# Kernel optimization log

Hardware: AMD Instinct MI355X
Metric: run time of the kernel (lower is better)

## Reference

```python
import jax, jax.numpy as jnp
import numpy as np

N_MOLS = 2048       # number of molecules (segments)
BOND_FDIM = 14      # slice last BOND_FDIM columns of f_bonds
DEPTH = 3


def setup_inputs() -> dict:
    key = jax.random.key(0)
    ks = jax.random.split(key, 12)
    n_atoms, n_bonds = 65536, 131072
    atom_fdim, bond_total, hidden, max_nb = 133, 147, 256, 6
    atom_features = jax.random.normal(ks[0], (n_atoms, atom_fdim), jnp.float32)
    f_bonds = jax.random.normal(ks[1], (n_bonds, bond_total), jnp.float32)
    a2a = jax.random.randint(ks[2], (n_atoms, max_nb), 0, n_atoms, jnp.int32)
    a2b = jax.random.randint(ks[3], (n_atoms, max_nb), 0, n_bonds, jnp.int32)
    segment_ids = jnp.sort(jax.random.randint(ks[4], (n_atoms,), 0, N_MOLS, jnp.int32))
    s = 0.05
    Wi = jax.random.normal(ks[5], (atom_fdim, hidden), jnp.float32) * s
    bi = jax.random.normal(ks[6], (hidden,), jnp.float32) * s
    Wh = jax.random.normal(ks[7], (hidden + BOND_FDIM, hidden), jnp.float32) * s
    bh = jax.random.normal(ks[8], (hidden,), jnp.float32) * s
    Wo = jax.random.normal(ks[9], (atom_fdim + hidden, hidden), jnp.float32) * s
    bo = jax.random.normal(ks[10], (hidden,), jnp.float32) * s
    return {"atom_features": atom_features, "f_bonds": f_bonds, "a2a": a2a,
            "a2b": a2b, "segment_ids": segment_ids,
            "Wi": Wi, "bi": bi, "Wh": Wh, "bh": bh, "Wo": Wo, "bo": bo}


def reference(atom_features, f_bonds, a2a, a2b, segment_ids, Wi, bi, Wh, bh, Wo, bo):
    # W_i + ReLU
    inp = atom_features @ Wi + bi                      # [N, H]
    message = jax.nn.relu(inp)
    fb = f_bonds[:, -BOND_FDIM:]                       # slice last bond_fdim cols
    # depth-1 message passing steps
    for _ in range(DEPTH - 1):
        nei_a_sum = message[a2a].sum(axis=1)           # [N, H]   gather + sum
        nei_b_sum = fb[a2b].sum(axis=1)                # [N, Fb]  gather + sum
        # sum(concat) == concat(sums) over neighbor axis
        m = jnp.concatenate([nei_a_sum, nei_b_sum], axis=1) @ Wh + bh
        message = jax.nn.relu(inp + m)                 # dropout: eval mode (identity)
    # final atom readout
    a_message = message[a2a].sum(axis=1)               # [N, H]
    a_input = jnp.concatenate([atom_features, a_message], axis=1)
    atom_hiddens = jax.nn.relu(a_input @ Wo + bo)      # [N, H]
    # segment-mean pooling over molecules (empty segments -> zero vector)
    sums = jax.ops.segment_sum(atom_hiddens, segment_ids, num_segments=N_MOLS)
    counts = jax.ops.segment_sum(jnp.ones((atom_hiddens.shape[0],), atom_hiddens.dtype),
                                 segment_ids, num_segments=N_MOLS)
    vecs = jnp.where(counts[:, None] > 0, sums / jnp.maximum(counts, 1.0)[:, None], 0.0)
    return vecs
```

## Files before the change

kernel.cpp:

```cpp
#include <hip/hip_runtime.h>

#define N_ATOMS 65536
#define AF      133
#define BT      147
#define HID     256
#define NNB     6
#define NM      2048

#define KI   160
#define KB   32
#define KP   256
#define LSI  168
#define LSB  40
#define LSP  264

#define BM   32

typedef __attribute__((ext_vector_type(8))) short short8;
typedef __attribute__((ext_vector_type(4))) float f32x4;

__device__ __forceinline__ unsigned short f2bf(float f) {
    unsigned u = __builtin_bit_cast(unsigned, f);
    u += 0x7fffu + ((u >> 16) & 1u);
    return (unsigned short)(u >> 16);
}
__device__ __forceinline__ float bf2f(unsigned short s) {
    unsigned u = ((unsigned)s) << 16;
    return __builtin_bit_cast(float, u);
}

__device__ __forceinline__ size_t fidx(int K, int n, int k) {
    return ((size_t)(((n >> 4) * (K >> 5) + (k >> 5)) * 64
                     + (((k >> 3) & 3) << 4) + (n & 15)) << 3) + (k & 7);
}

__global__ __launch_bounds__(256) void k_prep_bond(const float* __restrict__ Wi,
                                                   const float* __restrict__ Wh,
                                                   const float* __restrict__ Wo,
                                                   const float* __restrict__ bi,
                                                   const float* __restrict__ bh,
                                                   const float* __restrict__ f_bonds,
                                                   const int* __restrict__ a2b,
                                                   unsigned short* __restrict__ Wi_f,
                                                   unsigned short* __restrict__ Wb_f,
                                                   unsigned short* __restrict__ Whm_f,
                                                   unsigned short* __restrict__ Woa_f,
                                                   unsigned short* __restrict__ Wom_f,
                                                   unsigned short* __restrict__ bondsum,
                                                   float* __restrict__ b_ih) {
    if (blockIdx.x < 256) {
        const int n = blockIdx.x;
        if (n == 0) b_ih[threadIdx.x] = bi[threadIdx.x] + bh[threadIdx.x];
        for (int k = threadIdx.x; k < KI; k += 256) {
            Wi_f[fidx(KI, n, k)]  = f2bf(k < AF ? Wi[k * HID + n] : 0.f);
            Woa_f[fidx(KI, n, k)] = f2bf(k < AF ? Wo[k * HID + n] : 0.f);
        }
        for (int k = threadIdx.x; k < KB; k += 256)
            Wb_f[fidx(KB, n, k)] = f2bf(k < 14 ? Wh[(HID + k) * HID + n] : 0.f);
        for (int k = threadIdx.x; k < KP; k += 256) {
            Whm_f[fidx(KP, n, k)] = f2bf(Wh[k * HID + n]);
            Wom_f[fidx(KP, n, k)] = f2bf(Wo[(AF + k) * HID + n]);
        }
    } else {
        const int id   = (blockIdx.x - 256) * 256 + threadIdx.x;
        const int atom = id >> 4;
        const int c    = id & 15;
        float s = 0.f;
        if (c < 14) {
            const int* nb = &a2b[atom * NNB];
#pragma unroll
            for (int t = 0; t < NNB; ++t)
                s += f_bonds[(size_t)nb[t] * BT + (BT - 14) + c];
        }
        bondsum[atom * 32 + c]      = f2bf(s);
        bondsum[atom * 32 + 16 + c] = 0;
    }
}

template<int K, int LS>
__device__ __forceinline__ void mfma_core_pf(const unsigned short* __restrict__ As,
                                             const unsigned short* __restrict__ Wt,
                                             f32x4 (&acc)[2][2], int cw, int lane) {
    constexpr int NK = K >> 5;
    const int lm = lane & 15, quad = lane >> 4;
    const short8* __restrict__ Wf = (const short8*)Wt;
    short8 bf[2][NK];
#pragma unroll
    for (int ks = 0; ks < NK; ++ks)
#pragma unroll
        for (int ct = 0; ct < 2; ++ct)
            bf[ct][ks] = Wf[(size_t)((cw * 2 + ct) * NK + ks) * 64 + lane];
#pragma unroll
    for (int ks = 0; ks < NK; ++ks) {
        short8 af[2];
#pragma unroll
        for (int rt = 0; rt < 2; ++rt)
            af[rt] = *(const short8*)&As[(rt * 16 + lm) * LS + ks * 32 + quad * 8];
#pragma unroll
        for (int rt = 0; rt < 2; ++rt)
#pragma unroll
            for (int ct = 0; ct < 2; ++ct)
                acc[rt][ct] = __builtin_amdgcn_mfma_f32_16x16x32_bf16(af[rt], bf[ct][ks], acc[rt][ct], 0, 0, 0);
    }
}

__device__ __forceinline__ void epi_to_lds(f32x4 (&acc)[2][2],
                                           const float* __restrict__ bias,
                                           bool relu_,
                                           unsigned short* __restrict__ E,
                                           int cw, int lane) {
    const int lm = lane & 15, quad = lane >> 4;
#pragma unroll
    for (int ct = 0; ct < 2; ++ct) {
        int col = cw * 32 + ct * 16 + lm;
        float bv = bias ? bias[col] : 0.f;
#pragma unroll
        for (int rt = 0; rt < 2; ++rt)
#pragma unroll
            for (int i = 0; i < 4; ++i) {
                float v = acc[rt][ct][i] + bv;
                if (relu_) v = fmaxf(v, 0.f);
                E[(rt * 16 + quad * 4 + i) * LSP + col] = f2bf(v);
            }
    }
}

template<int NT>
__device__ __forceinline__ void store_tile(unsigned short* __restrict__ dst, int base,
                                           const unsigned short* __restrict__ E, int tid) {
#pragma unroll
    for (int k = 0; k < BM * HID / (8 * NT); ++k) {
        int j = k * NT + tid;
        int r = j >> 5, g = j & 31;
        *(short8*)&dst[(size_t)(base + r) * HID + g * 8] = *(const short8*)&E[r * LSP + g * 8];
    }
}

__global__ __launch_bounds__(512, 6) void k_inp(const float* __restrict__ atom,
                                                const unsigned short* __restrict__ bondsum,
                                                const unsigned short* __restrict__ Wi_f,
                                                const unsigned short* __restrict__ Wb_f,
                                                const unsigned short* __restrict__ Whm_f,
                                                const unsigned short* __restrict__ Woa_f,
                                                const float* __restrict__ bi,
                                                const float* __restrict__ b_ih,
                                                const float* __restrict__ bo,
                                                unsigned short* __restrict__ P0,
                                                unsigned short* __restrict__ inp2,
                                                unsigned short* __restrict__ aw) {
    __shared__ unsigned short pool[BM * LSP * 2 + BM * LSB];
    unsigned short* X    = pool;
    unsigned short* work = pool + BM * LSP;
    unsigned short* bs   = pool + BM * LSP * 2;
    const int tid  = threadIdx.x;
    const int base = blockIdx.x * BM;

    for (int it = tid; it < BM * KI; it += 512) {
        int r = it / KI, c = it - r * KI;
        X[r * LSI + c] = f2bf(c < AF ? atom[(size_t)(base + r) * AF + c] : 0.f);
    }
    if (tid < BM * 4) {
        int r = tid >> 2, c = (tid & 3) * 8;
        *(short8*)&bs[r * LSB + c] = *(const short8*)&bondsum[(size_t)(base + r) * 32 + c];
    }
    __syncthreads();

    const int lane = tid & 63, cw = tid >> 6;
    f32x4 acc1[2][2] = {}, acc3[2][2] = {};
    mfma_core_pf<KI, LSI>(X, Wi_f, acc1, cw, lane);
    mfma_core_pf<KI, LSI>(X, Woa_f, acc3, cw, lane);
    __syncthreads();

    epi_to_lds(acc3, bo, false, X, cw, lane);
    epi_to_lds(acc1, bi, true, work, cw, lane);
    __syncthreads();

    store_tile<512>(aw, base, X, tid);
    f32x4 acc2[2][2] = {};
    mfma_core_pf<KP, LSP>(work, Whm_f, acc2, cw, lane);
    mfma_core_pf<KB, LSB>(bs, Wb_f, acc1, cw, lane);
    __syncthreads();

    epi_to_lds(acc2, nullptr, false, X, cw, lane);
    epi_to_lds(acc1, b_ih, false, work, cw, lane);
    __syncthreads();

    store_tile<512>(P0, base, X, tid);
    store_tile<512>(inp2, base, work, tid);
}

__global__ __launch_bounds__(512, 6) void k_it(const unsigned short* __restrict__ Pin,
                                               const unsigned short* __restrict__ base_,
                                               const int* __restrict__ a2a,
                                               const unsigned short* __restrict__ Wt,
                                               unsigned short* __restrict__ Pout) {
    __shared__ unsigned short mT[BM * LSP];
    __shared__ int nb_l[BM * NNB];
    const int tid  = threadIdx.x;
    const int base = blockIdx.x * BM;

    if (tid < BM * NNB) nb_l[tid] = a2a[base * NNB + tid];
    __syncthreads();

#pragma unroll
    for (int k = 0; k < 2; ++k) {
        int j = k * 512 + tid;
        int r = j >> 5, g = j & 31;
        const int* nb = &nb_l[r * NNB];
        float s[8] = {};
#pragma unroll
        for (int t = 0; t < NNB; ++t) {
            short8 u = *(const short8*)&Pin[(size_t)nb[t] * HID + g * 8];
#pragma unroll
            for (int q = 0; q < 8; ++q) s[q] += bf2f((unsigned short)u[q]);
        }
        short8 b = *(const short8*)&base_[(size_t)(base + r) * HID + g * 8];
        short8 o;
#pragma unroll
        for (int q = 0; q < 8; ++q)
            o[q] = (short)f2bf(fmaxf(s[q] + bf2f((unsigned short)b[q]), 0.f));
        *(short8*)&mT[r * LSP + g * 8] = o;
    }
    __syncthreads();

    const int lane = tid & 63, cw = tid >> 6;
    f32x4 acc[2][2] = {};
    mfma_core_pf<KP, LSP>(mT, Wt, acc, cw, lane);
    __syncthreads();
    epi_to_lds(acc, nullptr, false, mT, cw, lane);
    __syncthreads();
    store_tile<512>(Pout, base, mT, tid);
}

__global__ __launch_bounds__(256, 8) void k_gseg(const unsigned short* __restrict__ P,
                                                 const unsigned short* __restrict__ aw,
                                                 const int* __restrict__ a2a,
                                                 const int* __restrict__ seg,
                                                 float* __restrict__ out) {
    const int m = blockIdx.x;
    __shared__ int lohi[2];
    __shared__ float red[8 * 256];
    if (threadIdx.x == 0) {
        int lo = 0, hi = N_ATOMS;
        while (lo < hi) { int mid = (lo + hi) >> 1; if (seg[mid] < m) lo = mid + 1; else hi = mid; }
        lohi[0] = lo;
        int lo2 = lo, hi2 = N_ATOMS;
        while (lo2 < hi2) { int mid = (lo2 + hi2) >> 1; if (seg[mid] < m + 1) lo2 = mid + 1; else hi2 = mid; }
        lohi[1] = lo2;
    }
    __syncthreads();
    const int lo = lohi[0], hi = lohi[1];
    const int slot = threadIdx.x >> 5;
    const int cg   = threadIdx.x & 31;

    float s[8] = {};
#pragma unroll 1
    for (int i0 = lo; i0 < hi; i0 += 8) {
        int i = i0 + slot;
        if (i < hi) {
            const int* nb = &a2a[i * NNB];
            short8 a = *(const short8*)&aw[(size_t)i * HID + cg * 8];
            float v[8];
#pragma unroll
            for (int q = 0; q < 8; ++q) v[q] = bf2f((unsigned short)a[q]);
#pragma unroll
            for (int t = 0; t < NNB; ++t) {
                short8 u = *(const short8*)&P[(size_t)nb[t] * HID + cg * 8];
#pragma unroll
                for (int q = 0; q < 8; ++q) v[q] += bf2f((unsigned short)u[q]);
            }
#pragma unroll
            for (int q = 0; q < 8; ++q) s[q] += fmaxf(v[q], 0.f);
        }
    }
#pragma unroll
    for (int q = 0; q < 8; ++q) red[slot * 256 + cg * 8 + q] = s[q];
    __syncthreads();

    const int j = threadIdx.x;
    float tot = 0.f;
#pragma unroll
    for (int sl = 0; sl < 8; ++sl) tot += red[sl * 256 + j];
    const int cnt = hi - lo;
    out[m * HID + j] = (cnt > 0) ? (tot / (float)cnt) : 0.f;
}

extern "C" void kernel_launch(void* const* d_in, const int* in_sizes, int n_in,
                              void* d_out, int out_size, void* d_ws, size_t ws_size,
                              hipStream_t stream) {
    const float* atom    = (const float*)d_in[0];
    const float* f_bonds = (const float*)d_in[1];
    const int*   a2a     = (const int*)d_in[2];
    const int*   a2b     = (const int*)d_in[3];
    const int*   seg     = (const int*)d_in[4];
    const float* Wi      = (const float*)d_in[5];
    const float* bi      = (const float*)d_in[6];
    const float* Wh      = (const float*)d_in[7];
    const float* bh      = (const float*)d_in[8];
    const float* Wo      = (const float*)d_in[9];
    const float* bo      = (const float*)d_in[10];
    float* out = (float*)d_out;

    unsigned short* ws = (unsigned short*)d_ws;
    const size_t nh = (size_t)N_ATOMS * HID;
    unsigned short* Pa   = ws;
    unsigned short* Pb   = Pa + nh;
    unsigned short* inp2 = Pb + nh;
    unsigned short* aw   = inp2 + nh;
    unsigned short* bsum = aw + nh;
    unsigned short* Wi_f  = bsum + (size_t)N_ATOMS * 32;
    unsigned short* Wb_f  = Wi_f + 256 * KI;
    unsigned short* Whm_f = Wb_f + 256 * KB;
    unsigned short* Woa_f = Whm_f + 256 * KP;
    unsigned short* Wom_f = Woa_f + 256 * KI;
    float*          b_ih  = (float*)(Wom_f + 256 * KP);

    dim3 blk256(256), blk512(512);
    const int nbm = N_ATOMS / BM;

    k_prep_bond<<<256 + N_ATOMS * 16 / 256, blk256, 0, stream>>>(
        Wi, Wh, Wo, bi, bh, f_bonds, a2b,
        Wi_f, Wb_f, Whm_f, Woa_f, Wom_f, bsum, b_ih);
    k_inp<<<nbm, blk512, 0, stream>>>(atom, bsum, Wi_f, Wb_f, Whm_f, Woa_f,
                                      bi, b_ih, bo, Pa, inp2, aw);

    k_it<<<nbm, blk512, 0, stream>>>(Pa, inp2, a2a, Whm_f, Pb);
    k_it<<<nbm, blk512, 0, stream>>>(Pb, inp2, a2a, Wom_f, Pa);
    k_gseg<<<NM, blk256, 0, stream>>>(Pa, aw, a2a, seg, out);
}
```

Measured before the change: 317.7 us.

## Fuse bond-feature gather into input kernel and tune occupancy/unrolling

Moves the per-atom bond-feature gather-sum out of the prep kernel and into k_inp. The gather loads are issued early and reduced into LDS after the first GEMM epilogue, so their latency can overlap with the atom-feature load and the MFMA work. This drops the bondsum round trip through global memory and shrinks the prep launch to the weight conversion only. It also raises the k_it launch-bounds occupancy hint from 6 to 8 and unrolls the segment-pool loop by 2, which may increase register pressure or cause spills.

```diff
diff --git a/kernel.cpp b/kernel.cpp
--- a/kernel.cpp
+++ b/kernel.cpp
@@ -34,46 +34,28 @@
                      + (((k >> 3) & 3) << 4) + (n & 15)) << 3) + (k & 7);
 }
 
-__global__ __launch_bounds__(256) void k_prep_bond(const float* __restrict__ Wi,
-                                                   const float* __restrict__ Wh,
-                                                   const float* __restrict__ Wo,
-                                                   const float* __restrict__ bi,
-                                                   const float* __restrict__ bh,
-                                                   const float* __restrict__ f_bonds,
-                                                   const int* __restrict__ a2b,
-                                                   unsigned short* __restrict__ Wi_f,
-                                                   unsigned short* __restrict__ Wb_f,
-                                                   unsigned short* __restrict__ Whm_f,
-                                                   unsigned short* __restrict__ Woa_f,
-                                                   unsigned short* __restrict__ Wom_f,
-                                                   unsigned short* __restrict__ bondsum,
-                                                   float* __restrict__ b_ih) {
-    if (blockIdx.x < 256) {
-        const int n = blockIdx.x;
-        if (n == 0) b_ih[threadIdx.x] = bi[threadIdx.x] + bh[threadIdx.x];
-        for (int k = threadIdx.x; k < KI; k += 256) {
-            Wi_f[fidx(KI, n, k)]  = f2bf(k < AF ? Wi[k * HID + n] : 0.f);
-            Woa_f[fidx(KI, n, k)] = f2bf(k < AF ? Wo[k * HID + n] : 0.f);
-        }
-        for (int k = threadIdx.x; k < KB; k += 256)
-            Wb_f[fidx(KB, n, k)] = f2bf(k < 14 ? Wh[(HID + k) * HID + n] : 0.f);
-        for (int k = threadIdx.x; k < KP; k += 256) {
-            Whm_f[fidx(KP, n, k)] = f2bf(Wh[k * HID + n]);
-            Wom_f[fidx(KP, n, k)] = f2bf(Wo[(AF + k) * HID + n]);
-        }
-    } else {
-        const int id   = (blockIdx.x - 256) * 256 + threadIdx.x;
-        const int atom = id >> 4;
-        const int c    = id & 15;
-        float s = 0.f;
-        if (c < 14) {
-            const int* nb = &a2b[atom * NNB];
-#pragma unroll
-            for (int t = 0; t < NNB; ++t)
-                s += f_bonds[(size_t)nb[t] * BT + (BT - 14) + c];
-        }
-        bondsum[atom * 32 + c]      = f2bf(s);
-        bondsum[atom * 32 + 16 + c] = 0;
+__global__ __launch_bounds__(256) void k_prep(const float* __restrict__ Wi,
+                                              const float* __restrict__ Wh,
+                                              const float* __restrict__ Wo,
+                                              const float* __restrict__ bi,
+                                              const float* __restrict__ bh,
+                                              unsigned short* __restrict__ Wi_f,
+                                              unsigned short* __restrict__ Wb_f,
+                                              unsigned short* __restrict__ Whm_f,
+                                              unsigned short* __restrict__ Woa_f,
+                                              unsigned short* __restrict__ Wom_f,
+                                              float* __restrict__ b_ih) {
+    const int n = blockIdx.x;
+    if (n == 0) b_ih[threadIdx.x] = bi[threadIdx.x] + bh[threadIdx.x];
+    for (int k = threadIdx.x; k < KI; k += 256) {
+        Wi_f[fidx(KI, n, k)]  = f2bf(k < AF ? Wi[k * HID + n] : 0.f);
+        Woa_f[fidx(KI, n, k)] = f2bf(k < AF ? Wo[k * HID + n] : 0.f);
+    }
+    for (int k = threadIdx.x; k < KB; k += 256)
+        Wb_f[fidx(KB, n, k)] = f2bf(k < 14 ? Wh[(HID + k) * HID + n] : 0.f);
+    for (int k = threadIdx.x; k < KP; k += 256) {
+        Whm_f[fidx(KP, n, k)] = f2bf(Wh[k * HID + n]);
+        Wom_f[fidx(KP, n, k)] = f2bf(Wo[(AF + k) * HID + n]);
     }
 }
 
@@ -137,7 +119,8 @@
 }
 
 __global__ __launch_bounds__(512, 6) void k_inp(const float* __restrict__ atom,
-                                                const unsigned short* __restrict__ bondsum,
+                                                const float* __restrict__ f_bonds,
+                                                const int* __restrict__ a2b,
                                                 const unsigned short* __restrict__ Wi_f,
                                                 const unsigned short* __restrict__ Wb_f,
                                                 const unsigned short* __restrict__ Whm_f,
@@ -155,13 +138,27 @@
     const int tid  = threadIdx.x;
     const int base = blockIdx.x * BM;
 
+    const bool gact = tid < BM * 14;
+    const int  ga = tid / 14, gc = tid - ga * 14;
+    float gv[NNB];
+    if (gact) {
+        const int* nbp = &a2b[(size_t)(base + ga) * NNB];
+        int bidx[NNB];
+#pragma unroll
+        for (int t = 0; t < NNB; ++t) bidx[t] = nbp[t];
+#pragma unroll
+        for (int t = 0; t < NNB; ++t)
+            gv[t] = f_bonds[(size_t)bidx[t] * BT + (BT - 14) + gc];
+    }
+    __builtin_amdgcn_sched_barrier(0);
+
+    {
+        short8 zz = {};
+        if (tid < BM * LSB / 8) ((short8*)bs)[tid] = zz;
+    }
     for (int it = tid; it < BM * KI; it += 512) {
         int r = it / KI, c = it - r * KI;
         X[r * LSI + c] = f2bf(c < AF ? atom[(size_t)(base + r) * AF + c] : 0.f);
-    }
-    if (tid < BM * 4) {
-        int r = tid >> 2, c = (tid & 3) * 8;
-        *(short8*)&bs[r * LSB + c] = *(const short8*)&bondsum[(size_t)(base + r) * 32 + c];
     }
     __syncthreads();
 
@@ -173,6 +170,12 @@
 
     epi_to_lds(acc3, bo, false, X, cw, lane);
     epi_to_lds(acc1, bi, true, work, cw, lane);
+    if (gact) {
+        float s = 0.f;
+#pragma unroll
+        for (int t = 0; t < NNB; ++t) s += gv[t];
+        bs[ga * LSB + gc] = f2bf(s);
+    }
     __syncthreads();
 
     store_tile<512>(aw, base, X, tid);
@@ -189,7 +192,7 @@
     store_tile<512>(inp2, base, work, tid);
 }
 
-__global__ __launch_bounds__(512, 6) void k_it(const unsigned short* __restrict__ Pin,
+__global__ __launch_bounds__(512, 8) void k_it(const unsigned short* __restrict__ Pin,
                                                const unsigned short* __restrict__ base_,
                                                const int* __restrict__ a2a,
                                                const unsigned short* __restrict__ Wt,
@@ -254,7 +257,7 @@
     const int cg   = threadIdx.x & 31;
 
     float s[8] = {};
-#pragma unroll 1
+#pragma unroll 2
     for (int i0 = lo; i0 < hi; i0 += 8) {
         int i = i0 + slot;
         if (i < hi) {
@@ -307,8 +310,7 @@
     unsigned short* Pb   = Pa + nh;
     unsigned short* inp2 = Pb + nh;
     unsigned short* aw   = inp2 + nh;
-    unsigned short* bsum = aw + nh;
-    unsigned short* Wi_f  = bsum + (size_t)N_ATOMS * 32;
+    unsigned short* Wi_f  = aw + nh;
     unsigned short* Wb_f  = Wi_f + 256 * KI;
     unsigned short* Whm_f = Wb_f + 256 * KB;
     unsigned short* Woa_f = Whm_f + 256 * KP;
@@ -318,10 +320,10 @@
     dim3 blk256(256), blk512(512);
     const int nbm = N_ATOMS / BM;
 
-    k_prep_bond<<<256 + N_ATOMS * 16 / 256, blk256, 0, stream>>>(
-        Wi, Wh, Wo, bi, bh, f_bonds, a2b,
-        Wi_f, Wb_f, Whm_f, Woa_f, Wom_f, bsum, b_ih);
-    k_inp<<<nbm, blk512, 0, stream>>>(atom, bsum, Wi_f, Wb_f, Whm_f, Woa_f,
+    k_prep<<<256, blk256, 0, stream>>>(Wi, Wh, Wo, bi, bh,
+                                       Wi_f, Wb_f, Whm_f, Woa_f, Wom_f, b_ih);
+    k_inp<<<nbm, blk512, 0, stream>>>(atom, f_bonds, a2b,
+                                      Wi_f, Wb_f, Whm_f, Woa_f,
                                       bi, b_ih, bo, Pa, inp2, aw);
 
     k_it<<<nbm, blk512, 0, stream>>>(Pa, inp2, a2a, Whm_f, Pb);
```

After: 320.9 us. No clear change (+1.0%).
